# Optimization experiments

Measured on AMD Instinct MI355X. Metric: run time of the kernel, lower is better.

The kernel has to match this reference:

```python
import jax, jax.numpy as jnp
import numpy as np
from jax import lax

H = 32  # hidden_size


def setup_inputs() -> dict:
    key = jax.random.key(0)
    ks = jax.random.split(key, 8)
    B, T, I, O = 64, 16384, 1, 1
    s_ih = 1.0 / np.sqrt(H)
    inp = {
        "x": jax.random.normal(ks[0], (B, T, I), dtype=jnp.float32),
        # PyTorch nn.LSTM params: weight_ih_l0 [4H, I], weight_hh_l0 [4H, H], biases [4H]
        "W_ih": jax.random.uniform(ks[1], (4 * H, I), dtype=jnp.float32, minval=-s_ih, maxval=s_ih),
        "W_hh": jax.random.uniform(ks[2], (4 * H, H), dtype=jnp.float32, minval=-s_ih, maxval=s_ih),
        "b_ih": jax.random.uniform(ks[3], (4 * H,), dtype=jnp.float32, minval=-s_ih, maxval=s_ih),
        "b_hh": jax.random.uniform(ks[4], (4 * H,), dtype=jnp.float32, minval=-s_ih, maxval=s_ih),
        # Linear(H, O)
        "W_lin": jax.random.uniform(ks[5], (O, H), dtype=jnp.float32, minval=-s_ih, maxval=s_ih),
        "b_lin": jax.random.uniform(ks[6], (O,), dtype=jnp.float32, minval=-s_ih, maxval=s_ih),
    }
    return inp


def _lstm_seq(x, W_ih, W_hh, b_ih, b_hh):
    """Single-layer LSTM over (B, T, I) -> hidden sequence (B, T, H).
    PyTorch gate order: i, f, g, o."""
    B, T, _ = x.shape
    # Precompute input contribution for all timesteps: (B, T, 4H)
    xg = jnp.einsum("bti,gi->btg", x, W_ih) + (b_ih + b_hh)

    W_hh_T = W_hh.T  # (H, 4H)

    def step(carry, xg_t):
        h, c = carry  # each (B, H)
        gates = xg_t + h @ W_hh_T  # (B, 4H)
        i, f, g, o = jnp.split(gates, 4, axis=-1)
        i = jax.nn.sigmoid(i)
        f = jax.nn.sigmoid(f)
        g = jnp.tanh(g)
        o = jax.nn.sigmoid(o)
        c = f * c + i * g
        h = o * jnp.tanh(c)
        return (h, c), h

    h0 = jnp.zeros((B, H), dtype=x.dtype)
    c0 = jnp.zeros((B, H), dtype=x.dtype)
    _, hs = lax.scan(step, (h0, c0), jnp.swapaxes(xg, 0, 1))  # hs: (T, B, H)
    return jnp.swapaxes(hs, 0, 1)  # (B, T, H)


def reference(x, W_ih, W_hh, b_ih, b_hh, W_lin, b_lin):
    hs = _lstm_seq(x, W_ih, W_hh, b_ih, b_hh)  # (B, T, H)
    linear_out = jnp.einsum("bth,oh->bto", hs, W_lin) + b_lin  # (B, T, O)
    return x + linear_out  # residual skip connection
```

## Files before the change

kernel.cpp:

```cpp
#include <hip/hip_runtime.h>


#define HID 32
#define CHUNK 32

typedef float f2 __attribute__((ext_vector_type(2)));
typedef float f4 __attribute__((ext_vector_type(4)));
typedef unsigned int u32x2 __attribute__((ext_vector_type(2)));

#if defined(__has_builtin)
#if __has_builtin(__builtin_amdgcn_permlane32_swap)
#define HAVE_PLSWAP 1
#endif
#endif

__device__ __forceinline__ float rl(float v, int lane) {
    return __int_as_float(__builtin_amdgcn_readlane(__float_as_int(v), lane));
}

__device__ __forceinline__ float fsig(float v) {
    float e = __builtin_amdgcn_exp2f(v * -1.44269504088896340736f);
    return __builtin_amdgcn_rcpf(1.0f + e);
}
__device__ __forceinline__ float ftanh(float v) {
    float e = __builtin_amdgcn_exp2f(v * -2.88539008177792681472f);
    float r = __builtin_amdgcn_rcpf(1.0f + e);
    return __builtin_fmaf(2.0f, r, -1.0f);
}

__device__ __forceinline__ float cross_half(float p) {
#ifdef HAVE_PLSWAP
    const unsigned pu = __float_as_uint(p);
    u32x2 r = __builtin_amdgcn_permlane32_swap(pu, pu, false, false);
    return __uint_as_float(r[0] ^ r[1] ^ pu);
#else
    return __shfl_xor(p, 32, 64);
#endif
}

__global__ __launch_bounds__(64, 1)
void lstm_wave_scan(const float* __restrict__ x,
                    const float* __restrict__ W_ih,
                    const float* __restrict__ W_hh,
                    const float* __restrict__ b_ih,
                    const float* __restrict__ b_hh,
                    const float* __restrict__ W_lin,
                    const float* __restrict__ b_lin,
                    float* __restrict__ out,
                    int T) {
    __shared__ float h_hist[CHUNK][65];

    const int lane = threadIdx.x;
    const int j    = lane & 31;
    const int half = lane >> 5;
    const int b    = blockIdx.x;

    const int row1 = j + (half << 5);
    const int row2 = 64 + j + (half << 5);

    f2 w1[16], w2[16];
    {
        const f4* R1 = (const f4*)(W_hh + row1 * HID);
        const f4* R2 = (const f4*)(W_hh + row2 * HID);
#pragma unroll
        for (int m = 0; m < 8; ++m) {
            f4 v;
            v = R1[m]; w1[2*m] = {v.x, v.y}; w1[2*m+1] = {v.z, v.w};
            v = R2[m]; w2[2*m] = {v.x, v.y}; w2[2*m+1] = {v.z, v.w};
        }
    }
    const float wih1 = W_ih[row1], bb1 = b_ih[row1] + b_hh[row1];
    const float wih2 = W_ih[row2], bb2 = b_ih[row2] + b_hh[row2];

    const float pa = half ? -1.44269504088896340736f : -2.88539008177792681472f;
    const float pb = half ? 1.0f : 2.0f;
    const float pc = half ? 0.0f : -1.0f;

    const float blin = b_lin[0];

    float c = 0.0f;
    float h = 0.0f;

    const float* xb = x   + (size_t)b * T;
    float*       ob = out + (size_t)b * T;

    float xv = xb[j];

    for (int t0 = 0; t0 < T; t0 += CHUNK) {
        int t0n = t0 + CHUNK; if (t0n >= T) t0n = 0;
        float xv_next = xb[t0n + j];

#pragma unroll 8
        for (int tt = 0; tt < CHUNK; ++tt) {
            const float sx = rl(xv, tt);

            f2 acc1 = { __builtin_fmaf(sx, wih1, bb1), 0.0f };
            f2 acc2 = { __builtin_fmaf(sx, wih2, bb2), 0.0f };
#pragma unroll
            for (int m = 0; m < 16; ++m) {
                f2 hm = { rl(h, 32 + 2*m), rl(h, 32 + 2*m + 1) };
                acc1 = __builtin_elementwise_fma(w1[m], hm, acc1);
                acc2 = __builtin_elementwise_fma(w2[m], hm, acc2);
            }
            const float g1 = acc1.x + acc1.y;
            const float g2 = acc2.x + acc2.y;

            const float a1 = fsig(g1);
            const float e2 = __builtin_amdgcn_exp2f(g2 * pa);
            const float a2 = __builtin_fmaf(pb, __builtin_amdgcn_rcpf(1.0f + e2), pc);

            const float p = a1 * a2;
            const float q = cross_half(p);

            c = __builtin_fmaf(a1, c, q);
            h = a2 * ftanh(c);

            h_hist[tt][lane] = h;
        }

        {
            float facc = 0.0f;
#pragma unroll
            for (int k = 0; k < 32; ++k)
                facc = __builtin_fmaf(W_lin[k], h_hist[j][32 + k], facc);
            if (half == 0)
                ob[t0 + j] = xv + facc + blin;
        }

        xv = xv_next;
    }
}

extern "C" void kernel_launch(void* const* d_in, const int* in_sizes, int n_in,
                              void* d_out, int out_size, void* d_ws, size_t ws_size,
                              hipStream_t stream) {
    const float* x     = (const float*)d_in[0];
    const float* W_ih  = (const float*)d_in[1];
    const float* W_hh  = (const float*)d_in[2];
    const float* b_ih  = (const float*)d_in[3];
    const float* b_hh  = (const float*)d_in[4];
    const float* W_lin = (const float*)d_in[5];
    const float* b_lin = (const float*)d_in[6];
    float* out = (float*)d_out;

    const int B = 64;
    const int T = in_sizes[0] / B;

    dim3 grid(B);
    dim3 block(64);
    lstm_wave_scan<<<grid, block, 0, stream>>>(x, W_ih, W_hh, b_ih, b_hh,
                                               W_lin, b_lin, out, T);
}
```

Measured before the change: 3.276 ms.

## Use packed fp16 dot2 for recurrent matvec with prescaled weights

Converts the recurrent weights to fp16 pairs, prescaled by the exp2 activation constants, and computes the hidden-state matvec with v_dot2 instructions on fp16 hidden values packed from readlane results. Four independent accumulators replace the two-wide vector accumulator to shorten dependency chains, and the time loop is fully unrolled. The aim is to cut the instruction count on the serial critical path of each step. The cost is reduced precision in the recurrence, which may accumulate error over 16384 steps, plus extra pack/shift work per readlane.

```diff
diff --git a/kernel.cpp b/kernel.cpp
--- a/kernel.cpp
+++ b/kernel.cpp
@@ -4,28 +4,32 @@
 #define HID 32
 #define CHUNK 32
 
-typedef float f2 __attribute__((ext_vector_type(2)));
-typedef float f4 __attribute__((ext_vector_type(4)));
+typedef _Float16 f16x2 __attribute__((ext_vector_type(2)));
 typedef unsigned int u32x2 __attribute__((ext_vector_type(2)));
 
 #if defined(__has_builtin)
 #if __has_builtin(__builtin_amdgcn_permlane32_swap)
 #define HAVE_PLSWAP 1
 #endif
+#if __has_builtin(__builtin_amdgcn_fdot2)
+#define HAVE_FDOT2 1
+#endif
 #endif
 
 __device__ __forceinline__ float rl(float v, int lane) {
     return __int_as_float(__builtin_amdgcn_readlane(__float_as_int(v), lane));
 }
+__device__ __forceinline__ unsigned rlu(unsigned v, int lane) {
+    return (unsigned)__builtin_amdgcn_readlane((int)v, lane);
+}
 
-__device__ __forceinline__ float fsig(float v) {
-    float e = __builtin_amdgcn_exp2f(v * -1.44269504088896340736f);
-    return __builtin_amdgcn_rcpf(1.0f + e);
-}
-__device__ __forceinline__ float ftanh(float v) {
-    float e = __builtin_amdgcn_exp2f(v * -2.88539008177792681472f);
-    float r = __builtin_amdgcn_rcpf(1.0f + e);
-    return __builtin_fmaf(2.0f, r, -1.0f);
+__device__ __forceinline__ float fdot2(f16x2 a, f16x2 b, float c) {
+#ifdef HAVE_FDOT2
+    return __builtin_amdgcn_fdot2(a, b, c, false);
+#else
+    return __builtin_fmaf((float)a.x, (float)b.x,
+           __builtin_fmaf((float)a.y, (float)b.y, c));
+#endif
 }
 
 __device__ __forceinline__ float cross_half(float p) {
@@ -58,27 +62,28 @@
     const int row1 = j + (half << 5);
     const int row2 = 64 + j + (half << 5);
 
-    f2 w1[16], w2[16];
-    {
-        const f4* R1 = (const f4*)(W_hh + row1 * HID);
-        const f4* R2 = (const f4*)(W_hh + row2 * HID);
+    const float S1 = -1.44269504088896340736f;
+    const float S2 = -2.88539008177792681472f;
+    const float sc2 = half ? S1 : S2;
+
+    f16x2 w1[16], w2[16];
 #pragma unroll
-        for (int m = 0; m < 8; ++m) {
-            f4 v;
-            v = R1[m]; w1[2*m] = {v.x, v.y}; w1[2*m+1] = {v.z, v.w};
-            v = R2[m]; w2[2*m] = {v.x, v.y}; w2[2*m+1] = {v.z, v.w};
-        }
+    for (int m = 0; m < 16; ++m) {
+        w1[m] = { (_Float16)(W_hh[row1 * HID + 2*m]     * S1),
+                  (_Float16)(W_hh[row1 * HID + 2*m + 1] * S1) };
+        w2[m] = { (_Float16)(W_hh[row2 * HID + 2*m]     * sc2),
+                  (_Float16)(W_hh[row2 * HID + 2*m + 1] * sc2) };
     }
-    const float wih1 = W_ih[row1], bb1 = b_ih[row1] + b_hh[row1];
-    const float wih2 = W_ih[row2], bb2 = b_ih[row2] + b_hh[row2];
+    const float wih1 = W_ih[row1] * S1,  bb1 = (b_ih[row1] + b_hh[row1]) * S1;
+    const float wih2 = W_ih[row2] * sc2, bb2 = (b_ih[row2] + b_hh[row2]) * sc2;
 
-    const float pa = half ? -1.44269504088896340736f : -2.88539008177792681472f;
     const float pb = half ? 1.0f : 2.0f;
     const float pc = half ? 0.0f : -1.0f;
 
     const float blin = b_lin[0];
 
     float c = 0.0f;
+    unsigned h16u = 0;
     float h = 0.0f;
 
     const float* xb = x   + (size_t)b * T;
@@ -90,31 +95,52 @@
         int t0n = t0 + CHUNK; if (t0n >= T) t0n = 0;
         float xv_next = xb[t0n + j];
 
-#pragma unroll 8
+#pragma unroll
         for (int tt = 0; tt < CHUNK; ++tt) {
             const float sx = rl(xv, tt);
 
-            f2 acc1 = { __builtin_fmaf(sx, wih1, bb1), 0.0f };
-            f2 acc2 = { __builtin_fmaf(sx, wih2, bb2), 0.0f };
+            float a1p0 = __builtin_fmaf(sx, wih1, bb1), a1p1 = 0.f, a1p2 = 0.f, a1p3 = 0.f;
+            float a2p0 = __builtin_fmaf(sx, wih2, bb2), a2p1 = 0.f, a2p2 = 0.f, a2p3 = 0.f;
+
 #pragma unroll
-            for (int m = 0; m < 16; ++m) {
-                f2 hm = { rl(h, 32 + 2*m), rl(h, 32 + 2*m + 1) };
-                acc1 = __builtin_elementwise_fma(w1[m], hm, acc1);
-                acc2 = __builtin_elementwise_fma(w2[m], hm, acc2);
+            for (int m = 0; m < 4; ++m) {
+                unsigned l0 = rlu(h16u, 32 + 8*m    ), l1 = rlu(h16u, 33 + 8*m);
+                unsigned l2 = rlu(h16u, 34 + 8*m    ), l3 = rlu(h16u, 35 + 8*m);
+                unsigned l4 = rlu(h16u, 36 + 8*m    ), l5 = rlu(h16u, 37 + 8*m);
+                unsigned l6 = rlu(h16u, 38 + 8*m    ), l7 = rlu(h16u, 39 + 8*m);
+                unsigned p0 = (l0 & 0xffffu) | (l1 << 16);
+                unsigned p1 = (l2 & 0xffffu) | (l3 << 16);
+                unsigned p2 = (l4 & 0xffffu) | (l5 << 16);
+                unsigned p3 = (l6 & 0xffffu) | (l7 << 16);
+                f16x2 h0 = __builtin_bit_cast(f16x2, p0);
+                f16x2 h1 = __builtin_bit_cast(f16x2, p1);
+                f16x2 h2 = __builtin_bit_cast(f16x2, p2);
+                f16x2 h3 = __builtin_bit_cast(f16x2, p3);
+                a1p0 = fdot2(w1[4*m + 0], h0, a1p0);
+                a2p0 = fdot2(w2[4*m + 0], h0, a2p0);
+                a1p1 = fdot2(w1[4*m + 1], h1, a1p1);
+                a2p1 = fdot2(w2[4*m + 1], h1, a2p1);
+                a1p2 = fdot2(w1[4*m + 2], h2, a1p2);
+                a2p2 = fdot2(w2[4*m + 2], h2, a2p2);
+                a1p3 = fdot2(w1[4*m + 3], h3, a1p3);
+                a2p3 = fdot2(w2[4*m + 3], h3, a2p3);
             }
-            const float g1 = acc1.x + acc1.y;
-            const float g2 = acc2.x + acc2.y;
+            const float g1 = (a1p0 + a1p1) + (a1p2 + a1p3);
+            const float g2 = (a2p0 + a2p1) + (a2p2 + a2p3);
 
-            const float a1 = fsig(g1);
-            const float e2 = __builtin_amdgcn_exp2f(g2 * pa);
-            const float a2 = __builtin_fmaf(pb, __builtin_amdgcn_rcpf(1.0f + e2), pc);
+            const float a1 = __builtin_amdgcn_rcpf(1.0f + __builtin_amdgcn_exp2f(g1));
+            const float a2 = __builtin_fmaf(pb,
+                               __builtin_amdgcn_rcpf(1.0f + __builtin_amdgcn_exp2f(g2)), pc);
 
             const float p = a1 * a2;
             const float q = cross_half(p);
 
             c = __builtin_fmaf(a1, c, q);
-            h = a2 * ftanh(c);
+            const float e = __builtin_amdgcn_exp2f(c * S2);
+            const float th = __builtin_fmaf(2.0f, __builtin_amdgcn_rcpf(1.0f + e), -1.0f);
+            h = a2 * th;
 
+            h16u = (unsigned)(unsigned short)__builtin_bit_cast(unsigned short, (_Float16)h);
             h_hist[tt][lane] = h;
         }
 
```

After: 5.981 ms. +82.6%, slower.
